# Performance work log

Hardware: AMD Instinct MI355X
Metric: run time of the kernel (lower is better)

The kernel has to match this reference:

```python
import jax, jax.numpy as jnp
import numpy as np

NEG_SLOPE = 0.2  # LeakyReLU slope used in the torch module


def setup_inputs() -> dict:
    key = jax.random.key(0)
    k1, k2, k3, k4 = jax.random.split(key, 4)
    B, W, K, E = 32, 128, 128, 256  # E = 2*window_size (gatv2 doubles embed_dim)
    x = jax.random.normal(k1, (B, W, K), dtype=jnp.float32)
    lin_w = jax.random.normal(k2, (E, 2 * W), dtype=jnp.float32) * 0.05
    lin_b = jnp.zeros((E,), dtype=jnp.float32)
    a = jax.random.normal(k3, (E, 1), dtype=jnp.float32) * 0.1
    bias = jax.random.normal(k4, (K, K), dtype=jnp.float32) * 0.1
    return {"x": x, "lin_w": lin_w, "lin_b": lin_b, "a": a, "bias": bias}


def reference(x, lin_w, lin_b, a, bias):
    # x: [B, window, K] -> permute to [B, K, window]
    xp = jnp.transpose(x, (0, 2, 1))
    Wd = xp.shape[-1]
    # lin(concat(v_i, v_j)) = v_i @ Wl^T + v_j @ Wr^T + b, avoiding the
    # explicit repeat_interleave/repeat/cat of the torch code (same math).
    Wl, Wr = lin_w[:, :Wd], lin_w[:, Wd:]
    left = jnp.einsum('bkw,ew->bke', xp, Wl)   # [B, K, E]
    right = jnp.einsum('bkw,ew->bke', xp, Wr)  # [B, K, E]
    h = left[:, :, None, :] + right[:, None, :, :] + lin_b  # [B, K, K, E]
    h = jnp.where(h >= 0, h, NEG_SLOPE * h)  # LeakyReLU(0.2)
    e = jnp.einsum('bije,eo->bij', h, a)     # matmul with a, squeeze -> [B, K, K]
    e = e + bias                             # use_bias=True
    att = jax.nn.softmax(e, axis=2)          # dropout=0 / eval -> identity
    out = jax.nn.sigmoid(jnp.einsum('bij,bjw->biw', att, xp))  # [B, K, W]
    return jnp.transpose(out, (0, 2, 1))     # [B, window, K]
```

## Files before the change

kernel.cpp:

```cpp
#include <hip/hip_runtime.h>


typedef float v2f __attribute__((ext_vector_type(2)));
typedef float v4f __attribute__((ext_vector_type(4)));
typedef short bf16x8 __attribute__((ext_vector_type(8)));

#define WS_A6  2097152
#define WS_A4  (2097152 + 256)

__device__ __forceinline__ unsigned pack_bf16x2(float a, float b) {
    unsigned ua = __builtin_bit_cast(unsigned, a);
    unsigned ub = __builtin_bit_cast(unsigned, b);
    ua = (ua + 0x7FFFu + ((ua >> 16) & 1u)) >> 16;
    ub = (ub + 0x7FFFu + ((ub >> 16) & 1u)) >> 16;
    return ua | (ub << 16);
}

__global__ __launch_bounds__(256) void k_linear(
    const float* __restrict__ x, const float* __restrict__ lin_w,
    const float* __restrict__ lin_b, const float* __restrict__ a,
    float* __restrict__ ws)
{
    __shared__ unsigned short xT[64 * 136];
    __shared__ float Ps[64 * 68];

    const int t = threadIdx.x;
    const int b = blockIdx.x, rt = blockIdx.y, kt = blockIdx.z;
    const int r0 = rt * 64, k0 = kt * 64;
    const bool isL = (rt < 4);

    if (b == 0 && rt == 0 && kt == 0) {
        float av = a[t];
        ws[WS_A6 + t] = 0.6f * av;
        ws[WS_A4 + t] = 0.4f * av;
    }

    {
        const float* xg = x + b * 16384 + k0;
        #pragma unroll
        for (int q = 0; q < 4; ++q) {
            const int idx = t + q * 256;
            const int wp = idx >> 4;
            const int k4 = (idx & 15) << 2;
            const v4f r0v = *(const v4f*)(xg + (2 * wp) * 128 + k4);
            const v4f r1v = *(const v4f*)(xg + (2 * wp + 1) * 128 + k4);
            const int g   = wp >> 2;
            const int off = (2 * wp) & 7;
            #pragma unroll
            for (int u = 0; u < 4; ++u) {
                const int kk = k4 + u;
                const int gs = g ^ ((kk >> 3) & 15);
                *(unsigned*)&xT[kk * 136 + (gs << 3) + off] = pack_bf16x2(r0v[u], r1v[u]);
            }
        }
    }
    __syncthreads();

    const int l = t & 63, wave = t >> 6;
    const int lr = l & 15, lg = l >> 4;
    const int rr_a = wave * 16 + lr;
    const int r_g  = r0 + rr_a;
    const float* Arow = isL ? (lin_w + (size_t)r_g * 256)
                            : (lin_w + (size_t)(r_g - 256) * 256 + 128);
    bf16x8 af[4];
    #pragma unroll
    for (int kc = 0; kc < 4; ++kc) {
        const v4f a0 = *(const v4f*)(Arow + kc * 32 + lg * 8);
        const v4f a1 = *(const v4f*)(Arow + kc * 32 + lg * 8 + 4);
        unsigned p0 = pack_bf16x2(a0[0], a0[1]), p1 = pack_bf16x2(a0[2], a0[3]);
        unsigned p2 = pack_bf16x2(a1[0], a1[1]), p3 = pack_bf16x2(a1[2], a1[3]);
        af[kc] = __builtin_bit_cast(bf16x8, (uint4){p0, p1, p2, p3});
    }

    v4f acc[4];
    #pragma unroll
    for (int nf = 0; nf < 4; ++nf) acc[nf] = (v4f){0.f, 0.f, 0.f, 0.f};
    #pragma unroll
    for (int nf = 0; nf < 4; ++nf) {
        const int kk = nf * 16 + lr;
        const int vr = (kk >> 3) & 15;
        #pragma unroll
        for (int kc = 0; kc < 4; ++kc) {
            const bf16x8 bfv = *(const bf16x8*)&xT[kk * 136 + (((kc * 4 + lg) ^ vr) << 3)];
            acc[nf] = __builtin_amdgcn_mfma_f32_16x16x32_bf16(af[kc], bfv, acc[nf], 0, 0, 0);
        }
    }

    #pragma unroll
    for (int nf = 0; nf < 4; ++nf)
        #pragma unroll
        for (int j = 0; j < 4; ++j)
            Ps[(wave * 16 + lg * 4 + j) * 68 + nf * 16 + lr] = acc[nf][j];
    __syncthreads();

    #pragma unroll
    for (int q = 0; q < 4; ++q) {
        const int idx = t + q * 256;
        const int rr = idx >> 4, k4 = (idx & 15) << 2;
        const float lb = isL ? lin_b[r0 + rr] : 0.f;
        const v4f v = *(const v4f*)&Ps[rr * 68 + k4];
        float* dst = ws + ((size_t)(b * 512 + r0 + rr) * 128 + k0 + k4);
        *(v4f*)dst = (v4f){v[0] + lb, v[1] + lb, v[2] + lb, v[3] + lb};
    }
}

__global__ __launch_bounds__(256, 1) void k_attn(
    const float* __restrict__ x, const float* __restrict__ bias,
    const float* __restrict__ ws, float* __restrict__ out)
{
    __shared__ float Rs[2][8192];
    __shared__ float Lt[256 * 16];
    __shared__ float att[16 * 132];
    __shared__ float as6[256], as4[256];

    const int t = threadIdx.x;
    const int b = blockIdx.x, it = blockIdx.y;
    const float* Pb = ws + (size_t)b * 65536;
    const float* Rsrc = Pb + 32768;

    v4f rx[8];
#define RLOAD(n_) do { const float* s_ = Rsrc + (n_) * 8192 + t * 4;  \
    _Pragma("unroll") for (int q = 0; q < 8; ++q)                     \
      rx[q] = *(const v4f*)(s_ + q * 1024); } while (0)

    RLOAD(0);

    {
        const float* Ls = Pb + it * 16;
        #pragma unroll
        for (int q = 0; q < 4; ++q) {
            const int idx = t + q * 256;
            const int e = idx >> 2, il4 = (idx & 3) * 4;
            *(v4f*)&Lt[e * 16 + il4] = *(const v4f*)(Ls + e * 128 + il4);
        }
    }
    as6[t] = ws[WS_A6 + t];
    as4[t] = ws[WS_A4 + t];

    const int jp = t & 31, iq = t >> 5;
    const int j0 = jp * 4, il0 = iq * 2;

    float acc0[4] = {}, acc1[4] = {};
    float dr[4] = {};
    float dl0 = 0.f, dl1 = 0.f;

    #pragma unroll 1
    for (int n = 0; n < 4; ++n) {
        float* rs = &Rs[n & 1][0];
        {
            float* d_ = rs + t * 4;
            #pragma unroll
            for (int q = 0; q < 8; ++q) *(v4f*)(d_ + q * 1024) = rx[q];
        }
        if (n < 3) RLOAD(n + 1);
        __syncthreads();

        const int eg0 = n * 64;
        #pragma unroll
        for (int g = 0; g < 16; ++g) {
            const int e0 = g * 4, eg = eg0 + e0;
            v4f rv[4]; float2 lv[4];
            #pragma unroll
            for (int u = 0; u < 4; ++u) {
                rv[u] = *(const v4f*)&rs[(e0 + u) * 128 + j0];
                lv[u] = *(const float2*)&Lt[(eg + u) * 16 + il0];
            }
            const v4f a6v = *(const v4f*)&as6[eg];
            const v4f a4v = *(const v4f*)&as4[eg];
            #pragma unroll
            for (int u = 0; u < 4; ++u) {
                const float a6u = a6v[u], a4u = a4v[u];
                const float l0 = lv[u].x, l1 = lv[u].y;
                dl0 = fmaf(a6u, l0, dl0);
                dl1 = fmaf(a6u, l1, dl1);
                #pragma unroll
                for (int jj = 0; jj < 4; ++jj) {
                    const float r = rv[u][jj];
                    dr[jj]   = fmaf(a6u, r, dr[jj]);
                    acc0[jj] = fmaf(a4u, fabsf(l0 + r), acc0[jj]);
                    acc1[jj] = fmaf(a4u, fabsf(l1 + r), acc1[jj]);
                }
            }
        }
    }
    __syncthreads();

    float* xT = &Rs[0][0];
    {
        const float* xg = x + b * 16384;
        #pragma unroll
        for (int q = 0; q < 16; ++q) {
            const int idx = t + q * 256;
            const int w = idx >> 5, j4 = (idx & 31) * 4;
            const int s = ((j4 >> 2) & 15) << 1;
            const v4f xv = *(const v4f*)(xg + w * 128 + j4);
            xT[(j4 + 0) * 128 + (w ^ s)] = xv[0];
            xT[(j4 + 1) * 128 + (w ^ s)] = xv[1];
            xT[(j4 + 2) * 128 + (w ^ s)] = xv[2];
            xT[(j4 + 3) * 128 + (w ^ s)] = xv[3];
        }
    }

    const int i0r = it * 16 + il0;
    float ev0[4], ev1[4];
    {
        const v4f b0 = *(const v4f*)(bias + (i0r + 0) * 128 + j0);
        const v4f b1 = *(const v4f*)(bias + (i0r + 1) * 128 + j0);
        #pragma unroll
        for (int jj = 0; jj < 4; ++jj) {
            ev0[jj] = acc0[jj] + dl0 + dr[jj] + b0[jj];
            ev1[jj] = acc1[jj] + dl1 + dr[jj] + b1[jj];
        }
    }
#define SOFTMAX_ROW(EV, ROW) do {                                               \
    float m_ = fmaxf(fmaxf(EV[0], EV[1]), fmaxf(EV[2], EV[3]));                 \
    _Pragma("unroll") for (int d_ = 1; d_ <= 16; d_ <<= 1)                      \
        m_ = fmaxf(m_, __shfl_xor(m_, d_));                                     \
    float p0 = __expf(EV[0] - m_), p1 = __expf(EV[1] - m_);                     \
    float p2 = __expf(EV[2] - m_), p3 = __expf(EV[3] - m_);                     \
    float s_ = p0 + p1 + p2 + p3;                                               \
    _Pragma("unroll") for (int d_ = 1; d_ <= 16; d_ <<= 1)                      \
        s_ += __shfl_xor(s_, d_);                                               \
    const float inv_ = 1.f / s_;                                                \
    *(v4f*)&att[(ROW) * 132 + j0] =                                             \
        (v4f){p0 * inv_, p1 * inv_, p2 * inv_, p3 * inv_}; } while (0)

    SOFTMAX_ROW(ev0, il0 + 0);
    SOFTMAX_ROW(ev1, il0 + 1);
    __syncthreads();

    const int iq2 = t & 3, wp = t >> 2;
    const int i4 = iq2 * 4, w0 = wp * 2;
    float o[2][4] = {};
    #pragma unroll 4
    for (int jc = 0; jc < 32; ++jc) {
        const int wx = w0 ^ ((jc & 15) << 1);
        v4f av[4]; v2f xv[4];
        #pragma unroll
        for (int q = 0; q < 4; ++q)
            av[q] = *(const v4f*)&att[(i4 + q) * 132 + jc * 4];
        #pragma unroll
        for (int u = 0; u < 4; ++u)
            xv[u] = *(const v2f*)&xT[(jc * 4 + u) * 128 + wx];
        #pragma unroll
        for (int u = 0; u < 4; ++u)
            #pragma unroll
            for (int q = 0; q < 4; ++q) {
                o[0][q] = fmaf(xv[u].x, av[q][u], o[0][q]);
                o[1][q] = fmaf(xv[u].y, av[q][u], o[1][q]);
            }
    }
    #pragma unroll
    for (int w = 0; w < 2; ++w) {
        v4f r;
        r[0] = 1.f / (1.f + __expf(-o[w][0]));
        r[1] = 1.f / (1.f + __expf(-o[w][1]));
        r[2] = 1.f / (1.f + __expf(-o[w][2]));
        r[3] = 1.f / (1.f + __expf(-o[w][3]));
        *(v4f*)(out + (size_t)b * 16384 + (w0 + w) * 128 + it * 16 + i4) = r;
    }
}

extern "C" void kernel_launch(void* const* d_in, const int* in_sizes, int n_in,
                              void* d_out, int out_size, void* d_ws, size_t ws_size,
                              hipStream_t stream) {
    const float* x     = (const float*)d_in[0];
    const float* lin_w = (const float*)d_in[1];
    const float* lin_b = (const float*)d_in[2];
    const float* a     = (const float*)d_in[3];
    const float* bias  = (const float*)d_in[4];
    float* ws  = (float*)d_ws;
    float* out = (float*)d_out;

    k_linear<<<dim3(32, 8, 2), 256, 0, stream>>>(x, lin_w, lin_b, a, ws);
    k_attn  <<<dim3(32, 8), 256, 0, stream>>>(x, bias, ws, out);
}
```

Before: 32.48 us.

## Split attention E-reduction across waves and use bf16 MFMA for att@x

Each wave now handles a quarter of the E dimension for all 16 rows and the partial scores are reduced through shared memory, so each thread reuses loaded L values across 8 rows instead of 2. The final att@x product moves from scalar FMAs on a transposed fp32 x to bf16 MFMA 16x16x32, with x and attention probabilities packed to bf16 in LDS. The minimum-blocks hint is dropped from launch bounds. This adds a cross-wave reduction step and loses precision by rounding to bf16 in the output matmul.

```diff
diff --git a/kernel.cpp b/kernel.cpp
--- a/kernel.cpp
+++ b/kernel.cpp
@@ -104,14 +104,20 @@
     }
 }
 
-__global__ __launch_bounds__(256, 1) void k_attn(
+#define RS0 0
+#define RS1 8192
+#define LT  16384
+#define A6  20480
+#define A4  20736
+#define DLR 20992
+#define DRR 21056
+#define ATT 21568
+
+__global__ __launch_bounds__(256) void k_attn(
     const float* __restrict__ x, const float* __restrict__ bias,
     const float* __restrict__ ws, float* __restrict__ out)
 {
-    __shared__ float Rs[2][8192];
-    __shared__ float Lt[256 * 16];
-    __shared__ float att[16 * 132];
-    __shared__ float as6[256], as4[256];
+    __shared__ __align__(16) float S[22656];
 
     const int t = threadIdx.x;
     const int b = blockIdx.x, it = blockIdx.y;
@@ -131,133 +137,167 @@
         for (int q = 0; q < 4; ++q) {
             const int idx = t + q * 256;
             const int e = idx >> 2, il4 = (idx & 3) * 4;
-            *(v4f*)&Lt[e * 16 + il4] = *(const v4f*)(Ls + e * 128 + il4);
-        }
-    }
-    as6[t] = ws[WS_A6 + t];
-    as4[t] = ws[WS_A4 + t];
-
-    const int jp = t & 31, iq = t >> 5;
-    const int j0 = jp * 4, il0 = iq * 2;
-
-    float acc0[4] = {}, acc1[4] = {};
-    float dr[4] = {};
-    float dl0 = 0.f, dl1 = 0.f;
+            *(v4f*)&S[LT + e * 16 + il4] = *(const v4f*)(Ls + e * 128 + il4);
+        }
+    }
+    S[A6 + t] = ws[WS_A6 + t];
+    S[A4 + t] = ws[WS_A4 + t];
+
+    const int l = t & 63, wv = t >> 6;
+    const int jl = l & 31, il = l >> 5;
+    const int j0e = jl * 4;
+
+    float acc[8][4] = {};
+    float dle[8] = {};
+    float dre[4] = {};
 
     #pragma unroll 1
-    for (int n = 0; n < 4; ++n) {
-        float* rs = &Rs[n & 1][0];
+    for (int c = 0; c < 4; ++c) {
+        const int cur = c & 1;
         {
-            float* d_ = rs + t * 4;
+            float* d_ = &S[RS0 + cur * 8192] + t * 4;
             #pragma unroll
             for (int q = 0; q < 8; ++q) *(v4f*)(d_ + q * 1024) = rx[q];
         }
-        if (n < 3) RLOAD(n + 1);
+        if (c < 3) RLOAD(c + 1);
         __syncthreads();
 
-        const int eg0 = n * 64;
-        #pragma unroll
-        for (int g = 0; g < 16; ++g) {
-            const int e0 = g * 4, eg = eg0 + e0;
-            v4f rv[4]; float2 lv[4];
+        const float* rs = &S[RS0 + cur * 8192];
+        #pragma unroll
+        for (int g = 0; g < 4; ++g) {
+            const int er = wv * 16 + g * 4;
+            const int eg = c * 64 + er;
+            v4f rv[4], lA[4], lB[4];
             #pragma unroll
             for (int u = 0; u < 4; ++u) {
-                rv[u] = *(const v4f*)&rs[(e0 + u) * 128 + j0];
-                lv[u] = *(const float2*)&Lt[(eg + u) * 16 + il0];
+                rv[u] = *(const v4f*)&rs[(er + u) * 128 + j0e];
+                lA[u] = *(const v4f*)&S[LT + (eg + u) * 16 + il * 8];
+                lB[u] = *(const v4f*)&S[LT + (eg + u) * 16 + il * 8 + 4];
             }
-            const v4f a6v = *(const v4f*)&as6[eg];
-            const v4f a4v = *(const v4f*)&as4[eg];
+            const v4f a6v = *(const v4f*)&S[A6 + eg];
+            const v4f a4v = *(const v4f*)&S[A4 + eg];
             #pragma unroll
             for (int u = 0; u < 4; ++u) {
                 const float a6u = a6v[u], a4u = a4v[u];
-                const float l0 = lv[u].x, l1 = lv[u].y;
-                dl0 = fmaf(a6u, l0, dl0);
-                dl1 = fmaf(a6u, l1, dl1);
                 #pragma unroll
-                for (int jj = 0; jj < 4; ++jj) {
-                    const float r = rv[u][jj];
-                    dr[jj]   = fmaf(a6u, r, dr[jj]);
-                    acc0[jj] = fmaf(a4u, fabsf(l0 + r), acc0[jj]);
-                    acc1[jj] = fmaf(a4u, fabsf(l1 + r), acc1[jj]);
+                for (int q = 0; q < 4; ++q) {
+                    const float la = lA[u][q], lb2 = lB[u][q];
+                    dle[q]     = fmaf(a6u, la,  dle[q]);
+                    dle[4 + q] = fmaf(a6u, lb2, dle[4 + q]);
+                    #pragma unroll
+                    for (int jj = 0; jj < 4; ++jj) {
+                        const float r = rv[u][jj];
+                        acc[q][jj]     = fmaf(a4u, fabsf(la  + r), acc[q][jj]);
+                        acc[4 + q][jj] = fmaf(a4u, fabsf(lb2 + r), acc[4 + q][jj]);
+                    }
                 }
+                #pragma unroll
+                for (int jj = 0; jj < 4; ++jj)
+                    dre[jj] = fmaf(a6u, rv[u][jj], dre[jj]);
             }
         }
     }
+
+    {
+        float* red = &S[RS0];
+        #pragma unroll
+        for (int q = 0; q < 8; ++q)
+            *(v4f*)&red[wv * 2048 + (il * 8 + q) * 128 + j0e] =
+                (v4f){acc[q][0], acc[q][1], acc[q][2], acc[q][3]};
+        if (jl == 0) {
+            *(v4f*)&S[DLR + wv * 16 + il * 8]     = (v4f){dle[0], dle[1], dle[2], dle[3]};
+            *(v4f*)&S[DLR + wv * 16 + il * 8 + 4] = (v4f){dle[4], dle[5], dle[6], dle[7]};
+        }
+        if (il == 0)
+            *(v4f*)&S[DRR + wv * 128 + j0e] = (v4f){dre[0], dre[1], dre[2], dre[3]};
+    }
+
+    v4f xr[16];
+    {
+        const float* xg = x + b * 16384;
+        #pragma unroll
+        for (int q = 0; q < 8; ++q) {
+            const int idx = t + q * 256;
+            const int w = idx >> 4, j8 = (idx & 15) * 8;
+            xr[2 * q]     = *(const v4f*)(xg + w * 128 + j8);
+            xr[2 * q + 1] = *(const v4f*)(xg + w * 128 + j8 + 4);
+        }
+    }
     __syncthreads();
 
-    float* xT = &Rs[0][0];
-    {
-        const float* xg = x + b * 16384;
-        #pragma unroll
-        for (int q = 0; q < 16; ++q) {
-            const int idx = t + q * 256;
-            const int w = idx >> 5, j4 = (idx & 31) * 4;
-            const int s = ((j4 >> 2) & 15) << 1;
-            const v4f xv = *(const v4f*)(xg + w * 128 + j4);
-            xT[(j4 + 0) * 128 + (w ^ s)] = xv[0];
-            xT[(j4 + 1) * 128 + (w ^ s)] = xv[1];
-            xT[(j4 + 2) * 128 + (w ^ s)] = xv[2];
-            xT[(j4 + 3) * 128 + (w ^ s)] = xv[3];
-        }
-    }
-
-    const int i0r = it * 16 + il0;
-    float ev0[4], ev1[4];
-    {
-        const v4f b0 = *(const v4f*)(bias + (i0r + 0) * 128 + j0);
-        const v4f b1 = *(const v4f*)(bias + (i0r + 1) * 128 + j0);
-        #pragma unroll
-        for (int jj = 0; jj < 4; ++jj) {
-            ev0[jj] = acc0[jj] + dl0 + dr[jj] + b0[jj];
-            ev1[jj] = acc1[jj] + dl1 + dr[jj] + b1[jj];
-        }
-    }
-#define SOFTMAX_ROW(EV, ROW) do {                                               \
-    float m_ = fmaxf(fmaxf(EV[0], EV[1]), fmaxf(EV[2], EV[3]));                 \
-    _Pragma("unroll") for (int d_ = 1; d_ <= 16; d_ <<= 1)                      \
-        m_ = fmaxf(m_, __shfl_xor(m_, d_));                                     \
-    float p0 = __expf(EV[0] - m_), p1 = __expf(EV[1] - m_);                     \
-    float p2 = __expf(EV[2] - m_), p3 = __expf(EV[3] - m_);                     \
-    float s_ = p0 + p1 + p2 + p3;                                               \
-    _Pragma("unroll") for (int d_ = 1; d_ <= 16; d_ <<= 1)                      \
-        s_ += __shfl_xor(s_, d_);                                               \
-    const float inv_ = 1.f / s_;                                                \
-    *(v4f*)&att[(ROW) * 132 + j0] =                                             \
-        (v4f){p0 * inv_, p1 * inv_, p2 * inv_, p3 * inv_}; } while (0)
-
-    SOFTMAX_ROW(ev0, il0 + 0);
-    SOFTMAX_ROW(ev1, il0 + 1);
+    unsigned* ubf = (unsigned*)&S[RS1];
+    #pragma unroll
+    for (int q = 0; q < 8; ++q) {
+        const int idx = t + q * 256;
+        const int w = idx >> 4, jh = (idx & 15) * 4;
+        const v4f x0 = xr[2 * q], x1 = xr[2 * q + 1];
+        uint4 pk;
+        pk.x = pack_bf16x2(x0[0], x0[1]);  pk.y = pack_bf16x2(x0[2], x0[3]);
+        pk.z = pack_bf16x2(x1[0], x1[1]);  pk.w = pack_bf16x2(x1[2], x1[3]);
+        *(uint4*)&ubf[w * 68 + jh] = pk;
+    }
+
+    {
+        const int jps = t & 31, iqs = t >> 5;
+        const int j0s = jps * 4, il0 = iqs * 2;
+        const int i0 = it * 16;
+        const float* red = &S[RS0];
+        v4f drs = *(const v4f*)&S[DRR + j0s];
+        drs += *(const v4f*)&S[DRR + 128 + j0s];
+        drs += *(const v4f*)&S[DRR + 256 + j0s];
+        drs += *(const v4f*)&S[DRR + 384 + j0s];
+        unsigned* attu = (unsigned*)&S[ATT];
+        #pragma unroll
+        for (int ii = 0; ii < 2; ++ii) {
+            const int i = il0 + ii;
+            v4f sm = *(const v4f*)&red[i * 128 + j0s];
+            sm += *(const v4f*)&red[2048 + i * 128 + j0s];
+            sm += *(const v4f*)&red[4096 + i * 128 + j0s];
+            sm += *(const v4f*)&red[6144 + i * 128 + j0s];
+            const float dls = S[DLR + i] + S[DLR + 16 + i] + S[DLR + 32 + i] + S[DLR + 48 + i];
+            const v4f bi = *(const v4f*)(bias + (i0 + i) * 128 + j0s);
+            float ev[4];
+            #pragma unroll
+            for (int jj = 0; jj < 4; ++jj) ev[jj] = sm[jj] + dls + drs[jj] + bi[jj];
+            float m_ = fmaxf(fmaxf(ev[0], ev[1]), fmaxf(ev[2], ev[3]));
+            #pragma unroll
+            for (int d = 1; d <= 16; d <<= 1) m_ = fmaxf(m_, __shfl_xor(m_, d));
+            float p0 = __expf(ev[0] - m_), p1 = __expf(ev[1] - m_);
+            float p2 = __expf(ev[2] - m_), p3 = __expf(ev[3] - m_);
+            float s_ = p0 + p1 + p2 + p3;
+            #pragma unroll
+            for (int d = 1; d <= 16; d <<= 1) s_ += __shfl_xor(s_, d);
+            const float inv = 1.f / s_;
+            attu[i * 68 + jps * 2]     = pack_bf16x2(p0 * inv, p1 * inv);
+            attu[i * 68 + jps * 2 + 1] = pack_bf16x2(p2 * inv, p3 * inv);
+        }
+    }
     __syncthreads();
 
-    const int iq2 = t & 3, wp = t >> 2;
-    const int i4 = iq2 * 4, w0 = wp * 2;
-    float o[2][4] = {};
-    #pragma unroll 4
-    for (int jc = 0; jc < 32; ++jc) {
-        const int wx = w0 ^ ((jc & 15) << 1);
-        v4f av[4]; v2f xv[4];
-        #pragma unroll
-        for (int q = 0; q < 4; ++q)
-            av[q] = *(const v4f*)&att[(i4 + q) * 132 + jc * 4];
-        #pragma unroll
-        for (int u = 0; u < 4; ++u)
-            xv[u] = *(const v2f*)&xT[(jc * 4 + u) * 128 + wx];
-        #pragma unroll
-        for (int u = 0; u < 4; ++u)
-            #pragma unroll
-            for (int q = 0; q < 4; ++q) {
-                o[0][q] = fmaf(xv[u].x, av[q][u], o[0][q]);
-                o[1][q] = fmaf(xv[u].y, av[q][u], o[1][q]);
+    {
+        const int lr = l & 15, lg = l >> 4;
+        const int i0 = it * 16;
+        const unsigned* attu = (const unsigned*)&S[ATT];
+        bf16x8 paf[4];
+        #pragma unroll
+        for (int kc = 0; kc < 4; ++kc)
+            paf[kc] = *(const bf16x8*)&attu[lr * 68 + kc * 16 + lg * 4];
+        #pragma unroll
+        for (int nf = 0; nf < 2; ++nf) {
+            const int wrow = wv * 32 + nf * 16 + lr;
+            v4f pacc = (v4f){0.f, 0.f, 0.f, 0.f};
+            #pragma unroll
+            for (int kc = 0; kc < 4; ++kc) {
+                const bf16x8 bv = *(const bf16x8*)&ubf[wrow * 68 + kc * 16 + lg * 4];
+                pacc = __builtin_amdgcn_mfma_f32_16x16x32_bf16(paf[kc], bv, pacc, 0, 0, 0);
             }
-    }
-    #pragma unroll
-    for (int w = 0; w < 2; ++w) {
-        v4f r;
-        r[0] = 1.f / (1.f + __expf(-o[w][0]));
-        r[1] = 1.f / (1.f + __expf(-o[w][1]));
-        r[2] = 1.f / (1.f + __expf(-o[w][2]));
-        r[3] = 1.f / (1.f + __expf(-o[w][3]));
-        *(v4f*)(out + (size_t)b * 16384 + (w0 + w) * 128 + it * 16 + i4) = r;
+            v4f r;
+            r[0] = 1.f / (1.f + __expf(-pacc[0]));
+            r[1] = 1.f / (1.f + __expf(-pacc[1]));
+            r[2] = 1.f / (1.f + __expf(-pacc[2]));
+            r[3] = 1.f / (1.f + __expf(-pacc[3]));
+            *(v4f*)(out + (size_t)b * 16384 + wrow * 128 + i0 + lg * 4) = r;
+        }
     }
 }
 
```

New measurement: 27.42 us. 1.18x faster.
